# Optimization experiments

Measured on AMD Instinct MI355X. Metric: run time of the kernel, lower is better.

Reference implementation:

```python
import jax, jax.numpy as jnp
import numpy as np

E = 65536      # num edges
T = 262144     # num triplets
H = 128        # hidden_channels
D = 64         # int_emb_size
C = 8          # basis_emb_size
NR = 6         # num_radial
NS = 7         # num_spherical
NB = 6         # len(bt_list) = num_BT + 1
BT_LIST = (-1, 0, 1, 2, 3, 4)
NBS = 1        # num_before_skip (also used for after-skip list in original code)


def setup_inputs() -> dict:
    key = jax.random.key(0)
    ks = iter(jax.random.split(key, 40))
    s = 0.05
    p = lambda shape: jax.random.normal(next(ks), shape, dtype=jnp.float32) * s
    inp = dict(
        x=jax.random.normal(next(ks), (E, H), dtype=jnp.float32),
        rbf=jax.random.normal(next(ks), (E, NR), dtype=jnp.float32),
        sbf=jax.random.normal(next(ks), (T, NS * NR), dtype=jnp.float32),
        idx_kj=jax.random.randint(next(ks), (T,), 0, E),
        idx_ji=jax.random.randint(next(ks), (T,), 0, E),
        bt=jax.random.randint(next(ks), (E,), 0, 5),
        lambda_d=1,
        alpha=jnp.float32(0.7),
        # per-branch stacked weights (6 branches)
        W_kj=p((NB, H, H)), b_kj=jnp.zeros((NB, H), jnp.float32),
        W_rbf1=p((NB, NR, C)), W_rbf2=p((NB, C, H)),
        W_sbf1=p((NB, NS * NR, C)), W_sbf2=p((NB, C, D)),
        W_down=p((NB, H, D)),
        W_ji=p((H, H)), b_ji=jnp.zeros((H,), jnp.float32),
        W_up=p((D, H)),
        rb1_w=p((NBS, H, H)), rb1_b=jnp.zeros((NBS, H), jnp.float32),
        rb2_w=p((NBS, H, H)), rb2_b=jnp.zeros((NBS, H), jnp.float32),
        W_lin=p((H, H)), b_lin=jnp.zeros((H,), jnp.float32),
        ra1_w=p((NBS, H, H)), ra1_b=jnp.zeros((NBS, H), jnp.float32),
        ra2_w=p((NBS, H, H)), ra2_b=jnp.zeros((NBS, H), jnp.float32),
    )
    return inp


def reference(x, rbf, sbf, idx_kj, idx_ji, bt, lambda_d, alpha,
              W_kj, b_kj, W_rbf1, W_rbf2, W_sbf1, W_sbf2, W_down,
              W_ji, b_ji, W_up, rb1_w, rb1_b, rb2_w, rb2_b,
              W_lin, b_lin, ra1_w, ra1_b, ra2_w, ra2_b):
    act = jax.nn.silu

    x_ji = act(x @ W_ji + b_ji)                                  # [E,H]

    # per-branch edge transforms, vectorized over the 6 branches (axis b)
    tmp = act(jnp.einsum('eh,bhg->beg', x, W_kj) + b_kj[:, None, :])   # [B,E,H]
    rbf_p = jnp.einsum('er,brc->bec', rbf, W_rbf1)                     # [B,E,C]
    rbf_p = jnp.einsum('bec,bcg->beg', rbf_p, W_rbf2)                  # [B,E,H]
    tmp = tmp * rbf_p
    down = act(jnp.einsum('beh,bhd->bed', tmp, W_down))                # [B,E,D]

    sbf_p = jnp.einsum('ts,bsc->btc', sbf, W_sbf1)                     # [B,T,C]
    sbf_p = jnp.einsum('btc,bcd->btd', sbf_p, W_sbf2)                  # [B,T,D]

    spe = down[:, idx_kj, :] * sbf_p                                   # [B,T,D]

    # last branch scattered with weight alpha
    x_kj_tot = alpha * jax.ops.segment_sum(spe[-1], idx_ji, num_segments=E)

    # per band-type masked scatter with weight (1 - alpha)
    bt_trip = bt[idx_kj]                                               # [T]
    for b, btv in enumerate(BT_LIST):
        m = (bt_trip == btv).astype(x.dtype)[:, None]
        x_kj_tot = x_kj_tot + (1.0 - alpha) * jax.ops.segment_sum(
            spe[b] * m, idx_ji, num_segments=E)

    x_kj = act(x_kj_tot @ W_up)                                        # [E,H]
    h = x_ji + x_kj
    for i in range(rb1_w.shape[0]):
        h = h + act(act(h @ rb1_w[i] + rb1_b[i]) @ rb2_w[i] + rb2_b[i])
    h = act(h @ W_lin + b_lin) + x
    for i in range(ra1_w.shape[0]):
        h = h + act(act(h @ ra1_w[i] + ra1_b[i]) @ ra2_w[i] + ra2_b[i])
    return h
```

## Files before the change

### kernel.cpp

```cpp
#include <hip/hip_runtime.h>
#include <hip/hip_bf16.h>
#include <stdint.h>

typedef __bf16 bf16_t;
typedef bf16_t bf16x8 __attribute__((ext_vector_type(8)));
typedef bf16_t bf16x2 __attribute__((ext_vector_type(2)));
typedef float f32x4 __attribute__((ext_vector_type(4)));

#define E_N 65536
#define T_N 262144
#define CAP 16
#define OVF_MAX T_N

__device__ __forceinline__ float silu_f(float v) {
  return v / (1.0f + __expf(-v));
}

__device__ __forceinline__ int permrow(int n) {
  return (n & ~31) | ((n & 1) << 4) | ((n & 30) >> 1);
}

__device__ __forceinline__ uint32_t pack_bf16(float a, float b) {
  union { bf16x2 h; uint32_t u; } u;
  u.h[0] = (bf16_t)a; u.h[1] = (bf16_t)b;
  return u.u;
}

__device__ __forceinline__ void g2l16(const void* g, void* l) {
  __builtin_amdgcn_global_load_lds(
      (const __attribute__((address_space(1))) void*)g,
      (__attribute__((address_space(3))) void*)l, 16, 0, 0);
}

template<int KI, int NTJ>
__device__ __forceinline__ void gemm_tile(const bf16_t* A, const bf16_t* B,
                                          int mb, int nb, int l16, int q,
                                          f32x4 (&acc)[2][NTJ]) {
#pragma unroll
  for (int kt = 0; kt < KI; ++kt) {
    const int sw = ((kt * 4 + q) ^ l16) << 3;
    bf16x8 a0 = *(const bf16x8*)(A + ((mb + l16) << 7) + sw);
    bf16x8 a1 = *(const bf16x8*)(A + ((mb + 16 + l16) << 7) + sw);
#pragma unroll
    for (int tj = 0; tj < NTJ; ++tj) {
      bf16x8 b = *(const bf16x8*)(B + ((nb + tj * 16 + l16) << 7) + sw);
      acc[0][tj] = __builtin_amdgcn_mfma_f32_16x16x32_bf16(a0, b, acc[0][tj], 0, 0, 0);
      acc[1][tj] = __builtin_amdgcn_mfma_f32_16x16x32_bf16(a1, b, acc[1][tj], 0, 0, 0);
    }
  }
}

template<int C4>
__device__ __forceinline__ void stage_x(bf16_t* dst, const float* src, int tid) {
  const float4* g = (const float4*)src;
#pragma unroll
  for (int i = tid; i < 64 * C4; i += 256) {
    const int row = i / C4, c4 = i % C4;
    float4 v = g[i];
    bf16_t t[4] = {(bf16_t)v.x, (bf16_t)v.y, (bf16_t)v.z, (bf16_t)v.w};
    *(uint2*)(dst + (row << 7) + ((((c4 >> 1) ^ (row & 15)) << 3) | ((c4 & 1) << 2))) =
        *(const uint2*)t;
  }
}

__global__ void prep_kernel(
    const float* __restrict__ W_ji, const float* __restrict__ W_kj,
    const float* __restrict__ W_down, const float* __restrict__ W_up,
    const float* __restrict__ rb1, const float* __restrict__ rb2,
    const float* __restrict__ W_lin, const float* __restrict__ ra1,
    const float* __restrict__ ra2, const float* __restrict__ W_rbf1,
    const float* __restrict__ W_rbf2, const float* __restrict__ x,
    char* __restrict__ wm_img, char* __restrict__ wdn_img,
    char* __restrict__ pset, bf16_t* __restrict__ wcb,
    bf16_t* __restrict__ ximg)
{
  __shared__ __align__(16) bf16_t tile[64 * 128];
  const int tid = threadIdx.x;
  const int blk = blockIdx.x;

  if (blk >= 115) {
    const int t = blk - 115;
    stage_x<32>(tile, x + (size_t)t * 8192, tid);
    __syncthreads();
    uint4* dst = (uint4*)(ximg + (size_t)t * 8192);
    const uint4* s = (const uint4*)tile;
#pragma unroll
    for (int i = 0; i < 4; ++i) dst[i * 256 + tid] = s[i * 256 + tid];
    return;
  }
  if (blk >= 112) {
    const int o = (blk - 112) * 256 + tid;
    if (o < 640) {
      const int b = o >> 7, n = o & 127;
      bf16_t t[8];
#pragma unroll
      for (int r = 0; r < 6; ++r) {
        const float* w1 = W_rbf1 + (b + 1) * 48 + r * 8;
        const float* w2 = W_rbf2 + (b + 1) * 1024 + n;
        float s = 0.f;
#pragma unroll
        for (int c = 0; c < 8; ++c) s += w1[c] * w2[c * 128];
        t[r] = (bf16_t)s;
      }
      t[6] = (bf16_t)0.f; t[7] = (bf16_t)0.f;
      *(uint4*)(wcb + (b * 128 + n) * 8) = *(const uint4*)t;
    }
    return;
  }
  if (blk >= 108) {
    const int item = (blk - 108) * 256 + tid;
    const int n = item >> 3, k8 = item & 7;
    bf16_t t[8];
#pragma unroll
    for (int j = 0; j < 8; ++j) t[j] = (bf16_t)W_up[(k8 * 8 + j) * 128 + n];
    const int row = permrow(n);
    *(uint4*)((bf16_t*)pset + (row << 7) + ((k8 ^ (row & 15)) << 3)) = *(const uint4*)t;
    return;
  }
  if (blk >= 88) {
    const int item = (blk - 88) * 256 + tid;
    const int m = item >> 10, w = item & 1023;
    const int n = w >> 4, k8 = w & 15;
    const float* src = W_down + (m + 1) * 8192;
    bf16_t* img = (bf16_t*)(wdn_img + m * 16384);
    bf16_t t[8];
#pragma unroll
    for (int j = 0; j < 8; ++j) t[j] = (bf16_t)src[(k8 * 8 + j) * 64 + n];
    const int row = permrow(n);
    *(uint4*)(img + (row << 7) + ((k8 ^ (row & 15)) << 3)) = *(const uint4*)t;
    return;
  }
  const int item = blk * 256 + tid;
  const int m = item >> 11, w = item & 2047;
  const int n = w >> 4, k8 = w & 15;
  const float* src; char* img;
  if (m == 0)      { src = W_ji;             img = wm_img; }
  else if (m <= 5) { src = W_kj + m * 16384; img = wm_img + m * 32768; }
  else if (m == 6) { src = rb1;   img = pset + 1 * 32768; }
  else if (m == 7) { src = rb2;   img = pset + 2 * 32768; }
  else if (m == 8) { src = W_lin; img = pset + 3 * 32768; }
  else if (m == 9) { src = ra1;   img = pset + 4 * 32768; }
  else             { src = ra2;   img = pset + 5 * 32768; }
  bf16_t t[8];
#pragma unroll
  for (int j = 0; j < 8; ++j) t[j] = (bf16_t)src[(k8 * 8 + j) * 128 + n];
  const int row = permrow(n);
  *(uint4*)((bf16_t*)img + (row << 7) + ((k8 ^ (row & 15)) << 3)) = *(const uint4*)t;
}

__global__ __launch_bounds__(256, 3)
void edge_kernel(const bf16_t* __restrict__ ximg, const float* __restrict__ rbf,
                 const float* __restrict__ b_kj, const float* __restrict__ b_ji,
                 const char* __restrict__ wm_img, const char* __restrict__ wdn_img,
                 const bf16_t* __restrict__ wcb,
                 bf16_t* __restrict__ x_ji_out, bf16_t* __restrict__ down)
{
  __shared__ __align__(16) bf16_t xA[64 * 128];
  __shared__ __align__(16) bf16_t Wb[128 * 128];
  __shared__ __align__(16) bf16_t wcbS[128 * 8];
  __shared__ __align__(16) bf16_t rbfS[64 * 8];
  __shared__ float biasS[128];

  const int tid = threadIdx.x;
  const int lane = tid & 63, wv = tid >> 6;
  const int q = lane >> 4, l16 = lane & 15;
  const int mb = (wv >> 1) * 32, nb = (wv & 1) * 64;
  const int eb = blockIdx.x;
  const int br = eb % 6;
  const int tile = eb / 6;
  const int R = tile * 64;

  {
    const char* xs = (const char*)(ximg + (size_t)tile * 8192);
    char* xd = (char*)xA;
#pragma unroll
    for (int c = 0; c < 4; ++c) {
      const int off = (c * 4 + wv) * 1024 + lane * 16;
      g2l16(xs + off, xd + off);
    }
    const char* wsrc = wm_img + (size_t)br * 32768;
    char* wd = (char*)Wb;
#pragma unroll
    for (int c = 0; c < 8; ++c) {
      const int off = (c * 4 + wv) * 1024 + lane * 16;
      g2l16(wsrc + off, wd + off);
    }
  }
  if (br == 0) {
    if (tid < 128) biasS[tid] = b_ji[tid];
  } else {
    if (tid < 128) biasS[tid] = b_kj[br * 128 + tid];
    if (wv < 2) {
      const char* cs = (const char*)(wcb + (size_t)(br - 1) * 1024);
      const int off = wv * 1024 + lane * 16;
      g2l16(cs + off, (char*)wcbS + off);
    }
    if (tid < 64) {
      const float* rg = rbf + (size_t)(R + tid) * 6;
      bf16_t t[8] = {(bf16_t)rg[0], (bf16_t)rg[1], (bf16_t)rg[2],
                     (bf16_t)rg[3], (bf16_t)rg[4], (bf16_t)rg[5],
                     (bf16_t)0.f, (bf16_t)0.f};
      *(uint4*)(rbfS + tid * 8) = *(const uint4*)t;
    }
  }
  __syncthreads();

  f32x4 acc[2][4] = {};
  gemm_tile<4, 4>(xA, Wb, mb, nb, l16, q, acc);

  if (br == 0) {
#pragma unroll
    for (int ti = 0; ti < 2; ++ti)
#pragma unroll
      for (int r = 0; r < 4; ++r) {
        const int row = mb + ti * 16 + q * 4 + r;
#pragma unroll
        for (int gl = 0; gl < 2; ++gl) {
          const int col0 = nb + gl * 32 + 2 * l16;
          const float2 b2 = *(const float2*)&biasS[col0];
          *(uint32_t*)&x_ji_out[(size_t)(R + row) * 128 + col0] =
              pack_bf16(silu_f(acc[ti][2 * gl][r] + b2.x),
                        silu_f(acc[ti][2 * gl + 1][r] + b2.y));
        }
      }
    return;
  }

  __syncthreads();

  {
    const char* ds = wdn_img + (size_t)(br - 1) * 16384;
    char* dd = (char*)Wb;
#pragma unroll
    for (int c = 0; c < 4; ++c) {
      const int off = (c * 4 + wv) * 1024 + lane * 16;
      g2l16(ds + off, dd + off);
    }
  }

  float wc[2][2][6];
#pragma unroll
  for (int gl = 0; gl < 2; ++gl)
#pragma unroll
    for (int j = 0; j < 2; ++j) {
      const int col = nb + gl * 32 + 2 * l16 + j;
      bf16x8 w8 = *(const bf16x8*)&wcbS[col * 8];
#pragma unroll
      for (int c = 0; c < 6; ++c) wc[gl][j][c] = (float)w8[c];
    }
#pragma unroll
  for (int ti = 0; ti < 2; ++ti)
#pragma unroll
    for (int r = 0; r < 4; ++r) {
      const int row = mb + ti * 16 + q * 4 + r;
      bf16x8 rv8 = *(const bf16x8*)&rbfS[row * 8];
      float rv[6];
#pragma unroll
      for (int c = 0; c < 6; ++c) rv[c] = (float)rv8[c];
#pragma unroll
      for (int gl = 0; gl < 2; ++gl) {
        const int col0 = nb + gl * 32 + 2 * l16;
        const float2 b2 = *(const float2*)&biasS[col0];
        float p0 = 0.f, p1 = 0.f;
#pragma unroll
        for (int c = 0; c < 6; ++c) {
          p0 += rv[c] * wc[gl][0][c];
          p1 += rv[c] * wc[gl][1][c];
        }
        const float v0 = silu_f(acc[ti][2 * gl][r] + b2.x) * p0;
        const float v1 = silu_f(acc[ti][2 * gl + 1][r] + b2.y) * p1;
        *(uint32_t*)&xA[(row << 7) + ((((col0 >> 3) ^ (row & 15)) << 3) | (col0 & 7))] =
            pack_bf16(v0, v1);
      }
    }
  __syncthreads();

  const int nb2 = (wv & 1) * 32;
  f32x4 acc2[2][2] = {};
  gemm_tile<4, 2>(xA, Wb, mb, nb2, l16, q, acc2);
#pragma unroll
  for (int ti = 0; ti < 2; ++ti)
#pragma unroll
    for (int r = 0; r < 4; ++r) {
      const int row = mb + ti * 16 + q * 4 + r;
      const int col0 = nb2 + 2 * l16;
      *(uint32_t*)&down[((size_t)(br - 1) * E_N + R + row) * 64 + col0] =
          pack_bf16(silu_f(acc2[ti][0][r]), silu_f(acc2[ti][1][r]));
    }
}

__global__ __launch_bounds__(256, 4)
void c8_kernel(const float* __restrict__ sbf, const int* __restrict__ idx_kj,
               const int* __restrict__ idx_ji, const int* __restrict__ bt,
               const float* __restrict__ Wsbf1,
               float* __restrict__ c8g, uint32_t* __restrict__ meta,
               int* __restrict__ cnt, int* __restrict__ list,
               int* __restrict__ ovf)
{
  __shared__ float s_sbf[64 * 44];
  __shared__ float s_W1[2016];
  __shared__ float s_c8[64 * 16];
  __shared__ int s_bs[64];

  const int tid = threadIdx.x;
  const int base = blockIdx.x * 64;

  for (int i = tid; i < 2016; i += 256) s_W1[i] = Wsbf1[i];
  if (tid < 64) {
    const int t = base + tid;
    const int kj = idx_kj[t];
    const int ji = idx_ji[t];
    const int bs = bt[kj] + 1;
    s_bs[tid] = bs;
    meta[t] = (uint32_t)kj | ((uint32_t)bs << 16);
    const int pos = atomicAdd(&cnt[ji], 1);
    if (pos < CAP) {
      list[ji * CAP + pos] = t;
    } else {
      const int o = atomicAdd(&ovf[0], 1);
      if (o < OVF_MAX) { ovf[2 + 2 * o] = t; ovf[2 + 2 * o + 1] = ji; }
    }
  }
  {
    const float2* sg = (const float2*)(sbf + (size_t)base * 42);
    for (int i = tid; i < 64 * 21; i += 256) {
      const int r = i / 21, c2 = i - r * 21;
      const float2 v = sg[i];
      s_sbf[r * 44 + c2 * 2] = v.x;
      s_sbf[r * 44 + c2 * 2 + 1] = v.y;
    }
  }
  __syncthreads();

  {
    const int i = tid >> 2;
    const int brr = (tid >> 1) & 1;
    const int cg = tid & 1;
    const int b = brr ? s_bs[i] : 5;
    const float* w = &s_W1[b * 336 + cg * 4];
    const float* sb = &s_sbf[i * 44];
    float a0 = 0.f, a1 = 0.f, a2 = 0.f, a3 = 0.f;
#pragma unroll
    for (int s = 0; s < 42; ++s) {
      const float sv = sb[s];
      const float* ws = w + s * 8;
      a0 += sv * ws[0]; a1 += sv * ws[1]; a2 += sv * ws[2]; a3 += sv * ws[3];
    }
    float* dc = &s_c8[i * 16 + brr * 8 + cg * 4];
    dc[0] = a0; dc[1] = a1; dc[2] = a2; dc[3] = a3;
  }
  __syncthreads();

  {
    const float4* s4 = (const float4*)s_c8;
    float4* g4 = (float4*)(c8g + (size_t)base * 16);
    g4[tid] = s4[tid];
  }
}

__global__ __launch_bounds__(256, 8)
void gather_kernel(const int* __restrict__ cnt, const int* __restrict__ list,
                   const uint32_t* __restrict__ meta, const float* __restrict__ c8g,
                   const float* __restrict__ Wsbf2, const bf16_t* __restrict__ down,
                   const float* __restrict__ alpha_p, const int* __restrict__ ovf,
                   float* __restrict__ xkj)
{
  __shared__ float sW2[3072];
  for (int i = threadIdx.x; i < 3072; i += 256) sW2[i] = Wsbf2[i];
  __syncthreads();

  const int e = blockIdx.x * 4 + (threadIdx.x >> 6);
  const int j = threadIdx.x & 63;
  const float alpha = alpha_p[0], oma = 1.f - alpha;
  const float* w5 = &sW2[5 * 512 + j];

  int n = cnt[e];
  if (n > CAP) n = CAP;

  int tk = 0; uint32_t mk = 0;
  if ((j & 15) < n) {
    tk = list[e * CAP + (j & 15)];
    mk = meta[tk];
  }

  float acc = 0.f;
  for (int k = 0; k < n; ++k) {
    const int t = __builtin_amdgcn_readfirstlane(__shfl(tk, k, 64));
    const uint32_t m = __builtin_amdgcn_readfirstlane(__shfl(mk, k, 64));
    const int kj = m & 0xffff;
    const int b  = m >> 16;
    const float g5 = (float)down[((size_t)4 * E_N + kj) * 64 + j];
    const float gb = (float)down[((size_t)(b - 1) * E_N + kj) * 64 + j];
    const float* cp = c8g + (size_t)t * 16;
    float d5 = 0.f, db = 0.f;
#pragma unroll
    for (int c = 0; c < 8; ++c) {
      d5 += cp[c]     * w5[c * 64];
      db += cp[8 + c] * sW2[b * 512 + c * 64 + j];
    }
    acc += alpha * g5 * d5 + oma * gb * db;
  }

  const int oc = ovf[0];
  for (int k = 0; k < oc; ++k) {
    const int ji = ovf[2 + 2 * k + 1];
    if (ji != e) continue;
    const int t = ovf[2 + 2 * k];
    const uint32_t m = meta[t];
    const int kj = m & 0xffff;
    const int b  = m >> 16;
    const float g5 = (float)down[((size_t)4 * E_N + kj) * 64 + j];
    const float gb = (float)down[((size_t)(b - 1) * E_N + kj) * 64 + j];
    const float* cp = c8g + (size_t)t * 16;
    float d5 = 0.f, db = 0.f;
#pragma unroll
    for (int c = 0; c < 8; ++c) {
      d5 += cp[c]     * w5[c * 64];
      db += cp[8 + c] * sW2[b * 512 + c * 64 + j];
    }
    acc += alpha * g5 * d5 + oma * gb * db;
  }

  xkj[(size_t)e * 64 + j] = acc;
}

__global__ __launch_bounds__(256, 3)
void epi_kernel(const float* __restrict__ x, const bf16_t* __restrict__ x_ji,
                const float* __restrict__ xkj, const char* __restrict__ pset,
                const float* __restrict__ rb1_b, const float* __restrict__ rb2_b,
                const float* __restrict__ lin_b, const float* __restrict__ ra1_b,
                const float* __restrict__ ra2_b,
                float* __restrict__ out)
{
  __shared__ __align__(16) bf16_t buf[64 * 128];
  __shared__ __align__(16) bf16_t Wb[128 * 128];
  __shared__ float biasS[2][128];

  const int tid = threadIdx.x;
  const int lane = tid & 63, wv = tid >> 6;
  const int q = lane >> 4, l16 = lane & 15;
  const int mb = (wv >> 1) * 32, nb = (wv & 1) * 64;
  const int R = blockIdx.x * 64;

#define DMA_W(SLOT) do {                                                         \
    const char* ps_ = pset + (size_t)(SLOT) * 32768;                             \
    char* wd_ = (char*)Wb;                                                       \
    _Pragma("unroll")                                                            \
    for (int c_ = 0; c_ < 8; ++c_) {                                             \
      const int off_ = (c_ * 4 + wv) * 1024 + lane * 16;                         \
      g2l16(ps_ + off_, wd_ + off_);                                             \
    }                                                                            \
  } while (0)

  stage_x<16>(buf, xkj + (size_t)R * 64, tid);
  DMA_W(0);
  __syncthreads();

  f32x4 hreg[2][4];
  {
    f32x4 acc[2][4] = {};
    gemm_tile<2, 4>(buf, Wb, mb, nb, l16, q, acc);
    __syncthreads();
#pragma unroll
    for (int ti = 0; ti < 2; ++ti)
#pragma unroll
      for (int r = 0; r < 4; ++r) {
        const int row = mb + ti * 16 + q * 4 + r;
#pragma unroll
        for (int gl = 0; gl < 2; ++gl) {
          const int col0 = nb + gl * 32 + 2 * l16;
          union { uint32_t u; bf16x2 h; } xj;
          xj.u = *(const uint32_t*)&x_ji[(size_t)(R + row) * 128 + col0];
          const float h0 = (float)xj.h[0] + silu_f(acc[ti][2 * gl][r]);
          const float h1 = (float)xj.h[1] + silu_f(acc[ti][2 * gl + 1][r]);
          hreg[ti][2 * gl][r] = h0;
          hreg[ti][2 * gl + 1][r] = h1;
          *(uint32_t*)&buf[(row << 7) + ((((col0 >> 3) ^ (row & 15)) << 3) | (col0 & 7))] =
              pack_bf16(h0, h1);
        }
      }
    DMA_W(1);
    if (tid < 128) biasS[0][tid] = rb1_b[tid];
    __syncthreads();
  }

#define EPI_STAGE(K, NEXTSLOT, NEXTBIAS, BODY)                                   \
  {                                                                              \
    f32x4 acc[2][4] = {};                                                        \
    gemm_tile<4, 4>(buf, Wb, mb, nb, l16, q, acc);                               \
    __syncthreads();                                                             \
    const float* bs_ = biasS[((K) - 1) & 1];                                     \
    _Pragma("unroll")                                                            \
    for (int ti = 0; ti < 2; ++ti)                                               \
      _Pragma("unroll")                                                          \
      for (int r = 0; r < 4; ++r) {                                              \
        const int row = mb + ti * 16 + q * 4 + r;                                \
        _Pragma("unroll")                                                        \
        for (int gl = 0; gl < 2; ++gl) {                                         \
          const int col0 = nb + gl * 32 + 2 * l16;                               \
          const float2 b2 = *(const float2*)&bs_[col0];                          \
          const float g0 = acc[ti][2 * gl][r] + b2.x;                            \
          const float g1 = acc[ti][2 * gl + 1][r] + b2.y;                        \
          BODY                                                                   \
        }                                                                        \
      }                                                                          \
    if ((K) < 5) {                                                               \
      DMA_W(NEXTSLOT);                                                           \
      if (tid < 128) biasS[(K) & 1][tid] = NEXTBIAS[tid];                        \
      __syncthreads();                                                           \
    }                                                                            \
  }

  EPI_STAGE(1, 2, rb2_b, {
    *(uint32_t*)&buf[(row << 7) + ((((col0 >> 3) ^ (row & 15)) << 3) | (col0 & 7))] =
        pack_bf16(silu_f(g0), silu_f(g1));
  })

  EPI_STAGE(2, 3, lin_b, {
    const float h0 = hreg[ti][2 * gl][r] + silu_f(g0);
    const float h1 = hreg[ti][2 * gl + 1][r] + silu_f(g1);
    hreg[ti][2 * gl][r] = h0; hreg[ti][2 * gl + 1][r] = h1;
    *(uint32_t*)&buf[(row << 7) + ((((col0 >> 3) ^ (row & 15)) << 3) | (col0 & 7))] =
        pack_bf16(h0, h1);
  })

  EPI_STAGE(3, 4, ra1_b, {
    const float2 xv = *(const float2*)&x[(size_t)(R + row) * 128 + col0];
    const float h0 = silu_f(g0) + xv.x;
    const float h1 = silu_f(g1) + xv.y;
    hreg[ti][2 * gl][r] = h0; hreg[ti][2 * gl + 1][r] = h1;
    *(uint32_t*)&buf[(row << 7) + ((((col0 >> 3) ^ (row & 15)) << 3) | (col0 & 7))] =
        pack_bf16(h0, h1);
  })

  EPI_STAGE(4, 5, ra2_b, {
    *(uint32_t*)&buf[(row << 7) + ((((col0 >> 3) ^ (row & 15)) << 3) | (col0 & 7))] =
        pack_bf16(silu_f(g0), silu_f(g1));
  })

  EPI_STAGE(5, 0, ra2_b, {
    float2 o;
    o.x = hreg[ti][2 * gl][r] + silu_f(g0);
    o.y = hreg[ti][2 * gl + 1][r] + silu_f(g1);
    *(float2*)&out[(size_t)(R + row) * 128 + col0] = o;
  })
#undef EPI_STAGE
#undef DMA_W
}

extern "C" void kernel_launch(void* const* d_in, const int* in_sizes, int n_in,
                              void* d_out, int out_size, void* d_ws, size_t ws_size,
                              hipStream_t stream)
{
  (void)in_sizes; (void)n_in; (void)out_size; (void)ws_size;
  const float* x      = (const float*)d_in[0];
  const float* rbf    = (const float*)d_in[1];
  const float* sbf    = (const float*)d_in[2];
  const int*   idx_kj = (const int*)d_in[3];
  const int*   idx_ji = (const int*)d_in[4];
  const int*   bt     = (const int*)d_in[5];
  const float* alpha  = (const float*)d_in[7];
  const float* W_kj   = (const float*)d_in[8];
  const float* b_kj   = (const float*)d_in[9];
  const float* W_rbf1 = (const float*)d_in[10];
  const float* W_rbf2 = (const float*)d_in[11];
  const float* W_sbf1 = (const float*)d_in[12];
  const float* W_sbf2 = (const float*)d_in[13];
  const float* W_down = (const float*)d_in[14];
  const float* W_ji   = (const float*)d_in[15];
  const float* b_ji   = (const float*)d_in[16];
  const float* W_up   = (const float*)d_in[17];
  const float* rb1_w  = (const float*)d_in[18];
  const float* rb1_b  = (const float*)d_in[19];
  const float* rb2_w  = (const float*)d_in[20];
  const float* rb2_b  = (const float*)d_in[21];
  const float* W_lin  = (const float*)d_in[22];
  const float* b_lin  = (const float*)d_in[23];
  const float* ra1_w  = (const float*)d_in[24];
  const float* ra1_b  = (const float*)d_in[25];
  const float* ra2_w  = (const float*)d_in[26];
  const float* ra2_b  = (const float*)d_in[27];

  char* ws = (char*)d_ws;
  bf16_t* down   = (bf16_t*)(ws);
  bf16_t* x_ji   = (bf16_t*)(ws + 41943040);
  float*  xkj    = (float*) (ws + 58720256);
  char*   wm_img = ws + 75497472;
  char*   wdn_img= ws + 75694080;
  char*   pset   = ws + 75776000;
  bf16_t* wcb    = (bf16_t*)(ws + 75972608);
  float*    c8g  = (float*)   (ws + 75982848);
  uint32_t* meta = (uint32_t*)(ws + 92760064);
  int*      list = (int*)     (ws + 93808640);
  int*      cnt  = (int*)     (ws + 98002944);
  int*      ovf  = (int*)     (ws + 98265088);
  bf16_t* ximg   = (bf16_t*)c8g;

  hipMemsetAsync(cnt, 0, 262144 + 8, stream);
  prep_kernel<<<1139, 256, 0, stream>>>(W_ji, W_kj, W_down, W_up, rb1_w, rb2_w,
                                        W_lin, ra1_w, ra2_w, W_rbf1, W_rbf2, x,
                                        wm_img, wdn_img, pset, wcb, ximg);
  edge_kernel<<<E_N / 64 * 6, 256, 0, stream>>>(ximg, rbf, b_kj, b_ji, wm_img,
                                                wdn_img, wcb, x_ji, down);
  c8_kernel<<<T_N / 64, 256, 0, stream>>>(sbf, idx_kj, idx_ji, bt, W_sbf1,
                                          c8g, meta, cnt, list, ovf);
  gather_kernel<<<E_N / 4, 256, 0, stream>>>(cnt, list, meta, c8g, W_sbf2,
                                             down, alpha, ovf, xkj);
  epi_kernel<<<E_N / 64, 256, 0, stream>>>(x, x_ji, xkj, pset,
                                           rb1_b, rb2_b, b_lin, ra1_b, ra2_b,
                                           (float*)d_out);
}
```

Measured before the change: 367.6 us.

## Merge c8 into prep kernel and fuse triplet gather into epilogue kernel

Folds the per-triplet sbf projection and bucketing work into the prep kernel as extra blocks, and moves the per-edge gather/reduction of triplet contributions into the epilogue kernel, which writes results directly into its shared-memory bf16 A tile. This removes two kernel launches and the fp32 xkj round trip through global memory. In exchange, the epilogue now does a serial gather loop per wave over 16 rows before its GEMMs, reads Wsbf2 from global instead of LDS, and the x image moves to a separate workspace region. The gather result is also rounded to bf16 earlier.

```diff
diff --git a/kernel.cpp b/kernel.cpp
--- a/kernel.cpp
+++ b/kernel.cpp
@@ -63,7 +63,8 @@
   }
 }
 
-__global__ void prep_kernel(
+__global__ __launch_bounds__(256, 4)
+void prep_c8_kernel(
     const float* __restrict__ W_ji, const float* __restrict__ W_kj,
     const float* __restrict__ W_down, const float* __restrict__ W_up,
     const float* __restrict__ rb1, const float* __restrict__ rb2,
@@ -72,24 +73,97 @@
     const float* __restrict__ W_rbf2, const float* __restrict__ x,
     char* __restrict__ wm_img, char* __restrict__ wdn_img,
     char* __restrict__ pset, bf16_t* __restrict__ wcb,
-    bf16_t* __restrict__ ximg)
+    bf16_t* __restrict__ ximg,
+    const float* __restrict__ sbf, const int* __restrict__ idx_kj,
+    const int* __restrict__ idx_ji, const int* __restrict__ bt,
+    const float* __restrict__ Wsbf1,
+    float* __restrict__ c8g, uint32_t* __restrict__ meta,
+    int* __restrict__ cnt, int* __restrict__ list,
+    int* __restrict__ ovf)
 {
-  __shared__ __align__(16) bf16_t tile[64 * 128];
+  __shared__ __align__(16) union {
+    bf16_t tile[64 * 128];
+    struct {
+      float s_sbf[64 * 44];
+      float s_W1[2016];
+      float s_c8[64 * 16];
+      int s_bs[64];
+    } c;
+  } S;
+
   const int tid = threadIdx.x;
   const int blk = blockIdx.x;
 
-  if (blk >= 115) {
-    const int t = blk - 115;
-    stage_x<32>(tile, x + (size_t)t * 8192, tid);
+  if (blk < 4096) {
+    const int base = blk * 64;
+
+    for (int i = tid; i < 2016; i += 256) S.c.s_W1[i] = Wsbf1[i];
+    if (tid < 64) {
+      const int t = base + tid;
+      const int kj = idx_kj[t];
+      const int ji = idx_ji[t];
+      const int bs = bt[kj] + 1;
+      S.c.s_bs[tid] = bs;
+      meta[t] = (uint32_t)kj | ((uint32_t)bs << 16);
+      const int pos = atomicAdd(&cnt[ji], 1);
+      if (pos < CAP) {
+        list[ji * CAP + pos] = t;
+      } else {
+        const int o = atomicAdd(&ovf[0], 1);
+        if (o < OVF_MAX) { ovf[2 + 2 * o] = t; ovf[2 + 2 * o + 1] = ji; }
+      }
+    }
+    {
+      const float2* sg = (const float2*)(sbf + (size_t)base * 42);
+      for (int i = tid; i < 64 * 21; i += 256) {
+        const int r = i / 21, c2 = i - r * 21;
+        const float2 v = sg[i];
+        S.c.s_sbf[r * 44 + c2 * 2] = v.x;
+        S.c.s_sbf[r * 44 + c2 * 2 + 1] = v.y;
+      }
+    }
+    __syncthreads();
+
+    {
+      const int i = tid >> 2;
+      const int brr = (tid >> 1) & 1;
+      const int cg = tid & 1;
+      const int b = brr ? S.c.s_bs[i] : 5;
+      const float* w = &S.c.s_W1[b * 336 + cg * 4];
+      const float* sb = &S.c.s_sbf[i * 44];
+      float a0 = 0.f, a1 = 0.f, a2 = 0.f, a3 = 0.f;
+#pragma unroll
+      for (int s = 0; s < 42; ++s) {
+        const float sv = sb[s];
+        const float* ws = w + s * 8;
+        a0 += sv * ws[0]; a1 += sv * ws[1]; a2 += sv * ws[2]; a3 += sv * ws[3];
+      }
+      float* dc = &S.c.s_c8[i * 16 + brr * 8 + cg * 4];
+      dc[0] = a0; dc[1] = a1; dc[2] = a2; dc[3] = a3;
+    }
+    __syncthreads();
+
+    {
+      const float4* s4 = (const float4*)S.c.s_c8;
+      float4* g4 = (float4*)(c8g + (size_t)base * 16);
+      g4[tid] = s4[tid];
+    }
+    return;
+  }
+
+  const int pblk = blk - 4096;
+  if (pblk >= 115) {
+    const int t = pblk - 115;
+    stage_x<32>(S.tile, x + (size_t)t * 8192, tid);
     __syncthreads();
     uint4* dst = (uint4*)(ximg + (size_t)t * 8192);
-    const uint4* s = (const uint4*)tile;
+    const uint4* s = (const uint4*)S.tile;
 #pragma unroll
     for (int i = 0; i < 4; ++i) dst[i * 256 + tid] = s[i * 256 + tid];
     return;
   }
-  if (blk >= 112) {
-    const int o = (blk - 112) * 256 + tid;
+  if (pblk >= 112) {
+    const int o = (pblk - 112) * 256 + tid;
     if (o < 640) {
       const int b = o >> 7, n = o & 127;
       bf16_t t[8];
@@ -107,8 +181,8 @@
     }
     return;
   }
-  if (blk >= 108) {
-    const int item = (blk - 108) * 256 + tid;
+  if (pblk >= 108) {
+    const int item = (pblk - 108) * 256 + tid;
     const int n = item >> 3, k8 = item & 7;
     bf16_t t[8];
 #pragma unroll
@@ -117,8 +191,8 @@
     *(uint4*)((bf16_t*)pset + (row << 7) + ((k8 ^ (row & 15)) << 3)) = *(const uint4*)t;
     return;
   }
-  if (blk >= 88) {
-    const int item = (blk - 88) * 256 + tid;
+  if (pblk >= 88) {
+    const int item = (pblk - 88) * 256 + tid;
     const int m = item >> 10, w = item & 1023;
     const int n = w >> 4, k8 = w & 15;
     const float* src = W_down + (m + 1) * 8192;
@@ -130,7 +204,7 @@
     *(uint4*)(img + (row << 7) + ((k8 ^ (row & 15)) << 3)) = *(const uint4*)t;
     return;
   }
-  const int item = blk * 256 + tid;
+  const int item = pblk * 256 + tid;
   const int m = item >> 11, w = item & 2047;
   const int n = w >> 4, k8 = w & 15;
   const float* src; char* img;
@@ -289,144 +363,13 @@
     }
 }
 
-__global__ __launch_bounds__(256, 4)
-void c8_kernel(const float* __restrict__ sbf, const int* __restrict__ idx_kj,
-               const int* __restrict__ idx_ji, const int* __restrict__ bt,
-               const float* __restrict__ Wsbf1,
-               float* __restrict__ c8g, uint32_t* __restrict__ meta,
-               int* __restrict__ cnt, int* __restrict__ list,
-               int* __restrict__ ovf)
-{
-  __shared__ float s_sbf[64 * 44];
-  __shared__ float s_W1[2016];
-  __shared__ float s_c8[64 * 16];
-  __shared__ int s_bs[64];
-
-  const int tid = threadIdx.x;
-  const int base = blockIdx.x * 64;
-
-  for (int i = tid; i < 2016; i += 256) s_W1[i] = Wsbf1[i];
-  if (tid < 64) {
-    const int t = base + tid;
-    const int kj = idx_kj[t];
-    const int ji = idx_ji[t];
-    const int bs = bt[kj] + 1;
-    s_bs[tid] = bs;
-    meta[t] = (uint32_t)kj | ((uint32_t)bs << 16);
-    const int pos = atomicAdd(&cnt[ji], 1);
-    if (pos < CAP) {
-      list[ji * CAP + pos] = t;
-    } else {
-      const int o = atomicAdd(&ovf[0], 1);
-      if (o < OVF_MAX) { ovf[2 + 2 * o] = t; ovf[2 + 2 * o + 1] = ji; }
-    }
-  }
-  {
-    const float2* sg = (const float2*)(sbf + (size_t)base * 42);
-    for (int i = tid; i < 64 * 21; i += 256) {
-      const int r = i / 21, c2 = i - r * 21;
-      const float2 v = sg[i];
-      s_sbf[r * 44 + c2 * 2] = v.x;
-      s_sbf[r * 44 + c2 * 2 + 1] = v.y;
-    }
-  }
-  __syncthreads();
-
-  {
-    const int i = tid >> 2;
-    const int brr = (tid >> 1) & 1;
-    const int cg = tid & 1;
-    const int b = brr ? s_bs[i] : 5;
-    const float* w = &s_W1[b * 336 + cg * 4];
-    const float* sb = &s_sbf[i * 44];
-    float a0 = 0.f, a1 = 0.f, a2 = 0.f, a3 = 0.f;
-#pragma unroll
-    for (int s = 0; s < 42; ++s) {
-      const float sv = sb[s];
-      const float* ws = w + s * 8;
-      a0 += sv * ws[0]; a1 += sv * ws[1]; a2 += sv * ws[2]; a3 += sv * ws[3];
-    }
-    float* dc = &s_c8[i * 16 + brr * 8 + cg * 4];
-    dc[0] = a0; dc[1] = a1; dc[2] = a2; dc[3] = a3;
-  }
-  __syncthreads();
-
-  {
-    const float4* s4 = (const float4*)s_c8;
-    float4* g4 = (float4*)(c8g + (size_t)base * 16);
-    g4[tid] = s4[tid];
-  }
-}
-
-__global__ __launch_bounds__(256, 8)
-void gather_kernel(const int* __restrict__ cnt, const int* __restrict__ list,
-                   const uint32_t* __restrict__ meta, const float* __restrict__ c8g,
-                   const float* __restrict__ Wsbf2, const bf16_t* __restrict__ down,
-                   const float* __restrict__ alpha_p, const int* __restrict__ ovf,
-                   float* __restrict__ xkj)
-{
-  __shared__ float sW2[3072];
-  for (int i = threadIdx.x; i < 3072; i += 256) sW2[i] = Wsbf2[i];
-  __syncthreads();
-
-  const int e = blockIdx.x * 4 + (threadIdx.x >> 6);
-  const int j = threadIdx.x & 63;
-  const float alpha = alpha_p[0], oma = 1.f - alpha;
-  const float* w5 = &sW2[5 * 512 + j];
-
-  int n = cnt[e];
-  if (n > CAP) n = CAP;
-
-  int tk = 0; uint32_t mk = 0;
-  if ((j & 15) < n) {
-    tk = list[e * CAP + (j & 15)];
-    mk = meta[tk];
-  }
-
-  float acc = 0.f;
-  for (int k = 0; k < n; ++k) {
-    const int t = __builtin_amdgcn_readfirstlane(__shfl(tk, k, 64));
-    const uint32_t m = __builtin_amdgcn_readfirstlane(__shfl(mk, k, 64));
-    const int kj = m & 0xffff;
-    const int b  = m >> 16;
-    const float g5 = (float)down[((size_t)4 * E_N + kj) * 64 + j];
-    const float gb = (float)down[((size_t)(b - 1) * E_N + kj) * 64 + j];
-    const float* cp = c8g + (size_t)t * 16;
-    float d5 = 0.f, db = 0.f;
-#pragma unroll
-    for (int c = 0; c < 8; ++c) {
-      d5 += cp[c]     * w5[c * 64];
-      db += cp[8 + c] * sW2[b * 512 + c * 64 + j];
-    }
-    acc += alpha * g5 * d5 + oma * gb * db;
-  }
-
-  const int oc = ovf[0];
-  for (int k = 0; k < oc; ++k) {
-    const int ji = ovf[2 + 2 * k + 1];
-    if (ji != e) continue;
-    const int t = ovf[2 + 2 * k];
-    const uint32_t m = meta[t];
-    const int kj = m & 0xffff;
-    const int b  = m >> 16;
-    const float g5 = (float)down[((size_t)4 * E_N + kj) * 64 + j];
-    const float gb = (float)down[((size_t)(b - 1) * E_N + kj) * 64 + j];
-    const float* cp = c8g + (size_t)t * 16;
-    float d5 = 0.f, db = 0.f;
-#pragma unroll
-    for (int c = 0; c < 8; ++c) {
-      d5 += cp[c]     * w5[c * 64];
-      db += cp[8 + c] * sW2[b * 512 + c * 64 + j];
-    }
-    acc += alpha * g5 * d5 + oma * gb * db;
-  }
-
-  xkj[(size_t)e * 64 + j] = acc;
-}
-
 __global__ __launch_bounds__(256, 3)
 void epi_kernel(const float* __restrict__ x, const bf16_t* __restrict__ x_ji,
-                const float* __restrict__ xkj, const char* __restrict__ pset,
+                const char* __restrict__ pset,
+                const int* __restrict__ cnt, const int* __restrict__ list,
+                const uint32_t* __restrict__ meta, const float* __restrict__ c8g,
+                const float* __restrict__ Wsbf2, const bf16_t* __restrict__ down,
+                const float* __restrict__ alpha_p, const int* __restrict__ ovf,
                 const float* __restrict__ rb1_b, const float* __restrict__ rb2_b,
                 const float* __restrict__ lin_b, const float* __restrict__ ra1_b,
                 const float* __restrict__ ra2_b,
@@ -452,8 +395,64 @@
     }                                                                            \
   } while (0)
 
-  stage_x<16>(buf, xkj + (size_t)R * 64, tid);
   DMA_W(0);
+
+  {
+    const int j = lane;
+    const float alpha = alpha_p[0], oma = 1.f - alpha;
+    float w5r[8];
+#pragma unroll
+    for (int c = 0; c < 8; ++c) w5r[c] = Wsbf2[5 * 512 + c * 64 + j];
+    const int oc = ovf[0];
+
+    for (int ee = 0; ee < 16; ++ee) {
+      const int row = wv * 16 + ee;
+      const int e = R + row;
+      int n = cnt[e];
+      if (n > CAP) n = CAP;
+      int tk = 0; uint32_t mk = 0;
+      if ((j & 15) < n) {
+        tk = list[e * CAP + (j & 15)];
+        mk = meta[tk];
+      }
+      float acc = 0.f;
+      for (int k = 0; k < n; ++k) {
+        const int t = __builtin_amdgcn_readfirstlane(__shfl(tk, k, 64));
+        const uint32_t m = __builtin_amdgcn_readfirstlane(__shfl(mk, k, 64));
+        const int kj = m & 0xffff;
+        const int b  = m >> 16;
+        const float g5 = (float)down[((size_t)4 * E_N + kj) * 64 + j];
+        const float gb = (float)down[((size_t)(b - 1) * E_N + kj) * 64 + j];
+        const float* cp = c8g + (size_t)t * 16;
+        float d5 = 0.f, db = 0.f;
+#pragma unroll
+        for (int c = 0; c < 8; ++c) {
+          d5 += cp[c]     * w5r[c];
+          db += cp[8 + c] * Wsbf2[b * 512 + c * 64 + j];
+        }
+        acc += alpha * g5 * d5 + oma * gb * db;
+      }
+      for (int k = 0; k < oc; ++k) {
+        const int ji = ovf[2 + 2 * k + 1];
+        if (ji != e) continue;
+        const int t = ovf[2 + 2 * k];
+        const uint32_t m = meta[t];
+        const int kj = m & 0xffff;
+        const int b  = m >> 16;
+        const float g5 = (float)down[((size_t)4 * E_N + kj) * 64 + j];
+        const float gb = (float)down[((size_t)(b - 1) * E_N + kj) * 64 + j];
+        const float* cp = c8g + (size_t)t * 16;
+        float d5 = 0.f, db = 0.f;
+#pragma unroll
+        for (int c = 0; c < 8; ++c) {
+          d5 += cp[c]     * w5r[c];
+          db += cp[8 + c] * Wsbf2[b * 512 + c * 64 + j];
+        }
+        acc += alpha * g5 * d5 + oma * gb * db;
+      }
+      buf[(row << 7) + ((((j >> 3) ^ (row & 15)) << 3) | (j & 7))] = (bf16_t)acc;
+    }
+  }
   __syncthreads();
 
   f32x4 hreg[2][4];
@@ -584,7 +583,7 @@
   char* ws = (char*)d_ws;
   bf16_t* down   = (bf16_t*)(ws);
   bf16_t* x_ji   = (bf16_t*)(ws + 41943040);
-  float*  xkj    = (float*) (ws + 58720256);
+  bf16_t* ximg   = (bf16_t*)(ws + 58720256);
   char*   wm_img = ws + 75497472;
   char*   wdn_img= ws + 75694080;
   char*   pset   = ws + 75776000;
@@ -594,19 +593,17 @@
   int*      list = (int*)     (ws + 93808640);
   int*      cnt  = (int*)     (ws + 98002944);
   int*      ovf  = (int*)     (ws + 98265088);
-  bf16_t* ximg   = (bf16_t*)c8g;
 
   hipMemsetAsync(cnt, 0, 262144 + 8, stream);
-  prep_kernel<<<1139, 256, 0, stream>>>(W_ji, W_kj, W_down, W_up, rb1_w, rb2_w,
-                                        W_lin, ra1_w, ra2_w, W_rbf1, W_rbf2, x,
-                                        wm_img, wdn_img, pset, wcb, ximg);
+  prep_c8_kernel<<<5235, 256, 0, stream>>>(W_ji, W_kj, W_down, W_up, rb1_w,
+                                           rb2_w, W_lin, ra1_w, ra2_w, W_rbf1,
+                                           W_rbf2, x, wm_img, wdn_img, pset,
+                                           wcb, ximg, sbf, idx_kj, idx_ji, bt,
+                                           W_sbf1, c8g, meta, cnt, list, ovf);
   edge_kernel<<<E_N / 64 * 6, 256, 0, stream>>>(ximg, rbf, b_kj, b_ji, wm_img,
                                                 wdn_img, wcb, x_ji, down);
-  c8_kernel<<<T_N / 64, 256, 0, stream>>>(sbf, idx_kj, idx_ji, bt, W_sbf1,
-                                          c8g, meta, cnt, list, ovf);
-  gather_kernel<<<E_N / 4, 256, 0, stream>>>(cnt, list, meta, c8g, W_sbf2,
-                                             down, alpha, ovf, xkj);
-  epi_kernel<<<E_N / 64, 256, 0, stream>>>(x, x_ji, xkj, pset,
+  epi_kernel<<<E_N / 64, 256, 0, stream>>>(x, x_ji, pset, cnt, list, meta,
+                                           c8g, W_sbf2, down, alpha, ovf,
                                            rb1_b, rb2_b, b_lin, ra1_b, ra2_b,
                                            (float*)d_out);
 }
```

After: 387.3 us. +5.3%, slower.
